# Performance work log

Measured on AMD Instinct MI355X. Metric: run time of the kernel, lower is better.

The kernel has to match this reference:

```python
import jax, jax.numpy as jnp
import numpy as np

B, S, D = 2, 4096, 512
H, DK, DV = 8, 64, 64
LN_EPS = 1e-5
ATTN_EPS = 1e-6


def layer_norm(x, g, b):
    mu = jnp.mean(x, axis=-1, keepdims=True)
    var = jnp.var(x, axis=-1, keepdims=True)
    return (x - mu) * jax.lax.rsqrt(var + LN_EPS) * g + b


def setup_inputs() -> dict:
    key = jax.random.key(0)
    ks = jax.random.split(key, 12)
    s = 1.0 / np.sqrt(D)
    inp = {
        "Q": jax.random.normal(ks[0], (B, S, D), jnp.float32),
        "K": jax.random.normal(ks[1], (B, S, D), jnp.float32),
        "V": jax.random.normal(ks[2], (B, S, D), jnp.float32),
        "W_q": jax.random.normal(ks[3], (D, H * DK), jnp.float32) * s,
        "W_k": jax.random.normal(ks[4], (D, H * DK), jnp.float32) * s,
        "W_v": jax.random.normal(ks[5], (D, H * DV), jnp.float32) * s,
        "W_o": jax.random.normal(ks[6], (H * DV, D), jnp.float32) * s,
        "ln1_g": jnp.ones((D,), jnp.float32),
        "ln1_b": jnp.zeros((D,), jnp.float32),
        "ln2_g": jnp.ones((D,), jnp.float32),
        "ln2_b": jnp.zeros((D,), jnp.float32),
        "w1": jax.random.normal(ks[7], (4 * D, D), jnp.float32) * s,  # torch Linear: (out, in)
        "b1": jnp.zeros((4 * D,), jnp.float32),
        "w2": jax.random.normal(ks[8], (D, 4 * D), jnp.float32) * (1.0 / np.sqrt(4 * D)),
        "b2": jnp.zeros((D,), jnp.float32),
    }
    return inp


def reference(Q, K, V, W_q, W_k, W_v, W_o, ln1_g, ln1_b, ln2_g, ln2_b, w1, b1, w2, b2):
    Qn = layer_norm(Q, ln1_g, ln1_b)
    # project and split heads: [B,S,H,dk] -> [B,H,S,dk]
    q = (Qn @ W_q).reshape(B, S, H, DK).transpose(0, 2, 1, 3)
    k = (K @ W_k).reshape(B, S, H, DK).transpose(0, 2, 1, 3)
    v = (V @ W_v).reshape(B, S, H, DV).transpose(0, 2, 1, 3)
    scores = jnp.einsum("bhqd,bhkd->bhqk", q, k) / (np.sqrt(DK) + ATTN_EPS)
    attn = jax.nn.softmax(scores, axis=-1)  # same as max-subtract softmax
    ctx = jnp.einsum("bhqk,bhkd->bhqd", attn, v)
    ctx = ctx.transpose(0, 2, 1, 3).reshape(B, S, H * DV)
    att_out = ctx @ W_o  # dropout = identity (eval)
    X = Q + att_out
    Xn = layer_norm(X, ln2_g, ln2_b)
    h = jax.nn.gelu(Xn @ w1.T + b1, approximate=False)
    ffn = h @ w2.T + b2
    return X + ffn
```

## Files before the change

kernel.cpp:

```cpp
#include <hip/hip_runtime.h>

typedef unsigned short u16;
typedef __attribute__((ext_vector_type(8))) short short8;
typedef __attribute__((ext_vector_type(4))) float f32x4;

struct __align__(8) us4 { u16 x, y, z, w; };
struct __align__(8) ui2 { unsigned x, y; };

#define CEXP (1.44269504089f / (8.0f + 1e-6f))

__device__ __forceinline__ u16 f2bf(float f) {
  unsigned u = __builtin_bit_cast(unsigned, f);
  unsigned r = (u + 0x7FFFu + ((u >> 16) & 1u)) >> 16;
  return (u16)r;
}

__device__ __forceinline__ unsigned pack_bf2_trunc(float a, float b) {
  return __builtin_amdgcn_perm(__builtin_bit_cast(unsigned, b),
                               __builtin_bit_cast(unsigned, a), 0x07060302u);
}

__device__ __forceinline__ void async_load16(const void* g, void* l) {
  __builtin_amdgcn_global_load_lds((const __attribute__((address_space(1))) void*)g,
                                   (__attribute__((address_space(3))) void*)l, 16, 0, 0);
}

__global__ void prep_weights(const float* __restrict__ Wq, const float* __restrict__ Wk,
                             const float* __restrict__ Wv, const float* __restrict__ Wo,
                             const float* __restrict__ w1, const float* __restrict__ w2,
                             u16* __restrict__ wqkvT, u16* __restrict__ woT,
                             u16* __restrict__ w1b, u16* __restrict__ w2b) {
  const int z = blockIdx.y;
  const int stride = gridDim.x * blockDim.x;
  const int i0 = blockIdx.x * blockDim.x + threadIdx.x;
  if (z < 4) {
    const float* src = z == 0 ? Wq : z == 1 ? Wk : z == 2 ? Wv : Wo;
    u16* dst = z < 3 ? wqkvT + z * 512 * 512 : woT;
    const float scale = (z == 0) ? CEXP : 1.0f;
    for (int i = i0; i < 512 * 512; i += stride) {
      int n = i >> 9, k = i & 511;
      dst[i] = f2bf(src[k * 512 + n] * scale);
    }
  } else {
    const float* src = z == 4 ? w1 : w2;
    u16* dst = z == 4 ? w1b : w2b;
    for (int i = i0; i < 2048 * 512; i += stride) dst[i] = f2bf(src[i]);
  }
}

template <bool KV>
__launch_bounds__(128)
__global__ void ln_cast(const float* __restrict__ X, const float* __restrict__ gw,
                        const float* __restrict__ bw, u16* __restrict__ Y,
                        const float* __restrict__ Kin, const float* __restrict__ Vin,
                        u16* __restrict__ Kb, u16* __restrict__ Vb) {
  const int row = blockIdx.x, t = threadIdx.x;
  const size_t base = (size_t)row * 512;
  float4 x = ((const float4*)(X + base))[t];
  float s = x.x + x.y + x.z + x.w;
  float ss = x.x * x.x + x.y * x.y + x.z * x.z + x.w * x.w;
#pragma unroll
  for (int off = 32; off > 0; off >>= 1) {
    s += __shfl_xor(s, off);
    ss += __shfl_xor(ss, off);
  }
  __shared__ float red[4];
  if ((t & 63) == 0) { red[(t >> 6) * 2] = s; red[(t >> 6) * 2 + 1] = ss; }
  __syncthreads();
  const float tot = red[0] + red[2], tss = red[1] + red[3];
  const float mu = tot * (1.0f / 512.0f);
  const float var = tss * (1.0f / 512.0f) - mu * mu;
  const float rs = rsqrtf(var + 1e-5f);
  float4 g4 = ((const float4*)gw)[t];
  float4 b4 = ((const float4*)bw)[t];
  us4 o;
  o.x = f2bf((x.x - mu) * rs * g4.x + b4.x);
  o.y = f2bf((x.y - mu) * rs * g4.y + b4.y);
  o.z = f2bf((x.z - mu) * rs * g4.z + b4.z);
  o.w = f2bf((x.w - mu) * rs * g4.w + b4.w);
  ((us4*)(Y + base))[t] = o;
  if constexpr (KV) {
    float4 k4 = ((const float4*)(Kin + base))[t];
    float4 v4 = ((const float4*)(Vin + base))[t];
    us4 ko, vo;
    ko.x = f2bf(k4.x); ko.y = f2bf(k4.y); ko.z = f2bf(k4.z); ko.w = f2bf(k4.w);
    vo.x = f2bf(v4.x); vo.y = f2bf(v4.y); vo.z = f2bf(v4.z); vo.w = f2bf(v4.w);
    ((us4*)(Kb + base))[t] = ko;
    ((us4*)(Vb + base))[t] = vo;
  }
}

__launch_bounds__(256, 3)
__global__ void gemm_qkv(const u16* __restrict__ Aq, const u16* __restrict__ Ak,
                         const u16* __restrict__ Av, const u16* __restrict__ Bt,
                         u16* __restrict__ qb, u16* __restrict__ kb, u16* __restrict__ vtb) {
  __shared__ __align__(16) u16 sA[128 * 32];
  __shared__ __align__(16) u16 sB[128 * 32];
  const int tid = threadIdx.x;
  const int wave = tid >> 6, lane = tid & 63;
  const int l15 = lane & 15, quad = lane >> 4;
  const int m0 = blockIdx.x * 128, n0 = blockIdx.y * 128;
  const int sel = n0 >> 9;
  const u16* A = sel == 0 ? Aq : sel == 1 ? Ak : Av;
  const int wm = (wave >> 1) * 64, wn = (wave & 1) * 64;
  const int u0 = wave * 64 + lane, u1 = u0 + 256;
  const int K = 512;

  const u16* a0 = A + (size_t)(m0 + (u0 >> 2)) * K + (u0 & 3) * 8;
  const u16* a1 = A + (size_t)(m0 + (u1 >> 2)) * K + (u1 & 3) * 8;
  const u16* b0 = Bt + (size_t)(n0 + (u0 >> 2)) * K + (u0 & 3) * 8;
  const u16* b1p = Bt + (size_t)(n0 + (u1 >> 2)) * K + (u1 & 3) * 8;

  f32x4 acc[4][4] = {};
  for (int k0 = 0; k0 < K; k0 += 32) {
    async_load16(a0 + k0, &sA[wave * 512]);
    async_load16(a1 + k0, &sA[2048 + wave * 512]);
    async_load16(b0 + k0, &sB[wave * 512]);
    async_load16(b1p + k0, &sB[2048 + wave * 512]);
    __syncthreads();
    short8 af[4], bfr[4];
#pragma unroll
    for (int i = 0; i < 4; i++)
      af[i] = *(const short8*)&sA[(wm + i * 16 + l15) * 32 + quad * 8];
#pragma unroll
    for (int j = 0; j < 4; j++)
      bfr[j] = *(const short8*)&sB[(wn + j * 16 + l15) * 32 + quad * 8];
#pragma unroll
    for (int i = 0; i < 4; i++)
#pragma unroll
      for (int j = 0; j < 4; j++)
        acc[i][j] = __builtin_amdgcn_mfma_f32_16x16x32_bf16(af[i], bfr[j], acc[i][j], 0, 0, 0);
    __syncthreads();
  }

#pragma unroll
  for (int i = 0; i < 4; i++) {
#pragma unroll
    for (int j = 0; j < 4; j++) {
      const int ocol = ((n0 + wn) & 511) + j * 16 + l15;
      const int row0 = m0 + wm + i * 16 + quad * 4;
      if (sel < 2) {
        u16* C = sel == 0 ? qb : kb;
#pragma unroll
        for (int r = 0; r < 4; r++) C[(size_t)(row0 + r) * 512 + ocol] = f2bf(acc[i][j][r]);
      } else {
        const int b = row0 >> 12, s0 = row0 & 4095;
        const int hh = ocol >> 6, cc = ocol & 63;
        us4 pk;
        pk.x = f2bf(acc[i][j][0]); pk.y = f2bf(acc[i][j][1]);
        pk.z = f2bf(acc[i][j][2]); pk.w = f2bf(acc[i][j][3]);
        *(us4*)&vtb[((size_t)((b * 8 + hh) * 64 + cc) << 12) + s0] = pk;
      }
    }
  }
}

template <int EP, int TN, int LB>
__launch_bounds__(256, LB)
__global__ void gemm_bt(const u16* __restrict__ A, const u16* __restrict__ Bt,
                        int M, int N, int K, void* __restrict__ Cp,
                        const float* __restrict__ bias, const float* __restrict__ res) {
  constexpr int MI = (TN == 128) ? 4 : 2;
  __shared__ __align__(16) u16 sA[128 * 32];
  __shared__ __align__(16) u16 sB[TN * 32];
  const int tid = threadIdx.x;
  const int wave = tid >> 6, lane = tid & 63;
  const int l15 = lane & 15, quad = lane >> 4;
  const int m0 = blockIdx.x * 128, n0 = blockIdx.y * TN;
  const int wm = (TN == 128) ? (wave >> 1) * 64 : wave * 32;
  const int wn = (TN == 128) ? (wave & 1) * 64 : 0;
  const int u0 = wave * 64 + lane, u1 = u0 + 256;

  const u16* a0 = A + (size_t)(m0 + (u0 >> 2)) * K + (u0 & 3) * 8;
  const u16* a1 = A + (size_t)(m0 + (u1 >> 2)) * K + (u1 & 3) * 8;
  const u16* b0 = Bt + (size_t)(n0 + (u0 >> 2)) * K + (u0 & 3) * 8;

  f32x4 acc[MI][4] = {};
  for (int k0 = 0; k0 < K; k0 += 32) {
    async_load16(a0 + k0, &sA[wave * 512]);
    async_load16(a1 + k0, &sA[2048 + wave * 512]);
    async_load16(b0 + k0, &sB[wave * 512]);
    if constexpr (TN == 128) {
      const u16* b1p = Bt + (size_t)(n0 + (u1 >> 2)) * K + (u1 & 3) * 8;
      async_load16(b1p + k0, &sB[2048 + wave * 512]);
    }
    __syncthreads();
    short8 af[MI], bfr[4];
#pragma unroll
    for (int i = 0; i < MI; i++)
      af[i] = *(const short8*)&sA[(wm + i * 16 + l15) * 32 + quad * 8];
#pragma unroll
    for (int j = 0; j < 4; j++)
      bfr[j] = *(const short8*)&sB[(wn + j * 16 + l15) * 32 + quad * 8];
#pragma unroll
    for (int i = 0; i < MI; i++)
#pragma unroll
      for (int j = 0; j < 4; j++)
        acc[i][j] = __builtin_amdgcn_mfma_f32_16x16x32_bf16(af[i], bfr[j], acc[i][j], 0, 0, 0);
    __syncthreads();
  }

#pragma unroll
  for (int i = 0; i < MI; i++) {
#pragma unroll
    for (int j = 0; j < 4; j++) {
      const int col = n0 + wn + j * 16 + l15;
      const int row0 = m0 + wm + i * 16 + quad * 4;
      if (EP == 2) {
        float* C = (float*)Cp;
#pragma unroll
        for (int r = 0; r < 4; r++) {
          size_t idx = (size_t)(row0 + r) * N + col;
          C[idx] = acc[i][j][r] + res[idx];
        }
      } else if (EP == 3) {
        u16* C = (u16*)Cp;
        const float bv = bias[col];
#pragma unroll
        for (int r = 0; r < 4; r++) {
          float xx = acc[i][j][r] + bv;
          float gl = 0.5f * xx * (1.0f + erff(xx * 0.70710678118f));
          C[(size_t)(row0 + r) * N + col] = f2bf(gl);
        }
      } else {
        float* C = (float*)Cp;
        const float bv = bias[col];
#pragma unroll
        for (int r = 0; r < 4; r++) {
          size_t idx = (size_t)(row0 + r) * N + col;
          C[idx] = acc[i][j][r] + bv + res[idx];
        }
      }
    }
  }
}

__launch_bounds__(256, 3)
__global__ void attn_kernel(const u16* __restrict__ qb, const u16* __restrict__ kb,
                            const u16* __restrict__ vtb, u16* __restrict__ ctx) {
  __shared__ __align__(16) u16 sK[2 * 128 * 32];
  __shared__ __align__(16) u16 sV[4 * 64 * 32];
  __shared__ __align__(16) u16 sP[4 * 32 * 40];
  const int tid = threadIdx.x;
  const int wave = tid >> 6, lane = tid & 63;
  const int l15 = lane & 15, quad = lane >> 4;
  const int bh = blockIdx.y, b = bh >> 3, h = bh & 7;
  const int q0 = blockIdx.x * 128;
  const size_t rb = (size_t)b * 4096;

  short8 qf[2][2];
#pragma unroll
  for (int mi = 0; mi < 2; mi++)
#pragma unroll
    for (int kk = 0; kk < 2; kk++) {
      int row = q0 + wave * 32 + mi * 16 + l15;
      qf[mi][kk] = *(const short8*)&qb[(rb + row) * 512 + h * 64 + kk * 32 + quad * 8];
    }

  f32x4 o_t[2][4] = {};
  float l_part[2] = {0.f, 0.f};
  u16* myP = &sP[wave * 32 * 40];

  for (int j0 = 0; j0 < 4096; j0 += 128) {
#pragma unroll
    for (int r = 0; r < 4; r++) {
      int u = r * 256 + wave * 64 + lane;
      int kk = u >> 9, key = (u >> 2) & 127, c8 = u & 3;
      async_load16(&kb[(rb + j0 + key) * 512 + h * 64 + kk * 32 + c8 * 8],
                   &sK[(r * 256 + wave * 64) * 8]);
    }
#pragma unroll
    for (int r = 0; r < 4; r++) {
      int u = r * 256 + wave * 64 + lane;
      int kk = u >> 8, vc = (u >> 2) & 63, c8 = u & 3;
      async_load16(&vtb[((size_t)(bh * 64 + vc)) * 4096 + j0 + kk * 32 + c8 * 8],
                   &sV[(r * 256 + wave * 64) * 8]);
    }
    __syncthreads();

#pragma unroll
    for (int kk = 0; kk < 4; kk++) {
#pragma unroll
      for (int nh = 0; nh < 2; nh++) {
        const int ni = kk * 2 + nh;
        short8 af0 = *(const short8*)&sK[(ni * 16 + l15) * 32 + quad * 8];
        short8 af1 = *(const short8*)&sK[4096 + (ni * 16 + l15) * 32 + quad * 8];
#pragma unroll
        for (int mi = 0; mi < 2; mi++) {
          f32x4 st = {};
          st = __builtin_amdgcn_mfma_f32_16x16x32_bf16(af0, qf[mi][0], st, 0, 0, 0);
          st = __builtin_amdgcn_mfma_f32_16x16x32_bf16(af1, qf[mi][1], st, 0, 0, 0);
          float p0 = exp2f(st[0]), p1 = exp2f(st[1]);
          float p2 = exp2f(st[2]), p3 = exp2f(st[3]);
          l_part[mi] += (p0 + p1) + (p2 + p3);
          ui2 w;
          w.x = pack_bf2_trunc(p0, p1);
          w.y = pack_bf2_trunc(p2, p3);
          *(ui2*)&myP[(mi * 16 + l15) * 40 + nh * 16 + quad * 4] = w;
        }
      }
      asm volatile("s_waitcnt lgkmcnt(0)" ::: "memory");
      short8 pf[2], vf[4];
#pragma unroll
      for (int mi = 0; mi < 2; mi++)
        pf[mi] = *(const short8*)&myP[(mi * 16 + l15) * 40 + quad * 8];
#pragma unroll
      for (int vi = 0; vi < 4; vi++)
        vf[vi] = *(const short8*)&sV[kk * 2048 + (vi * 16 + l15) * 32 + quad * 8];
#pragma unroll
      for (int mi = 0; mi < 2; mi++)
#pragma unroll
        for (int vi = 0; vi < 4; vi++)
          o_t[mi][vi] = __builtin_amdgcn_mfma_f32_16x16x32_bf16(vf[vi], pf[mi], o_t[mi][vi], 0, 0, 0);
    }
    __syncthreads();
  }

#pragma unroll
  for (int mi = 0; mi < 2; mi++) {
    float l = l_part[mi];
    l += __shfl_xor(l, 16);
    l += __shfl_xor(l, 32);
    const float inv = 1.0f / l;
    const int row = q0 + wave * 32 + mi * 16 + l15;
#pragma unroll
    for (int vi = 0; vi < 4; vi++) {
      us4 o;
      o.x = f2bf(o_t[mi][vi][0] * inv);
      o.y = f2bf(o_t[mi][vi][1] * inv);
      o.z = f2bf(o_t[mi][vi][2] * inv);
      o.w = f2bf(o_t[mi][vi][3] * inv);
      *(us4*)&ctx[(rb + row) * 512 + h * 64 + vi * 16 + quad * 4] = o;
    }
  }
}

extern "C" void kernel_launch(void* const* d_in, const int* in_sizes, int n_in,
                              void* d_out, int out_size, void* d_ws, size_t ws_size,
                              hipStream_t stream) {
  (void)in_sizes; (void)n_in; (void)out_size; (void)ws_size;
  const float* Q = (const float*)d_in[0];
  const float* K = (const float*)d_in[1];
  const float* V = (const float*)d_in[2];
  const float* W_q = (const float*)d_in[3];
  const float* W_k = (const float*)d_in[4];
  const float* W_v = (const float*)d_in[5];
  const float* W_o = (const float*)d_in[6];
  const float* ln1_g = (const float*)d_in[7];
  const float* ln1_b = (const float*)d_in[8];
  const float* ln2_g = (const float*)d_in[9];
  const float* ln2_b = (const float*)d_in[10];
  const float* w1 = (const float*)d_in[11];
  const float* b1 = (const float*)d_in[12];
  const float* w2 = (const float*)d_in[13];
  const float* b2 = (const float*)d_in[14];

  char* w = (char*)d_ws;
  const size_t MB = 1u << 20;
  u16* wqkvT = (u16*)(w);
  u16* woT = (u16*)(w + 3 * MB / 2);
  u16* w1b = (u16*)(w + 2 * MB);
  u16* w2b = (u16*)(w + 4 * MB);
  u16* Qn  = (u16*)(w + 6 * MB);
  u16* Kb  = (u16*)(w + 14 * MB);
  u16* Vb  = (u16*)(w + 22 * MB);
  u16* qb  = (u16*)(w + 30 * MB);
  u16* kb  = (u16*)(w + 38 * MB);
  u16* vtb = (u16*)(w + 46 * MB);
  u16* ctx = (u16*)(w + 54 * MB);
  float* X = (float*)(w + 62 * MB);
  u16* Xn  = (u16*)(w + 6 * MB);
  u16* hb  = (u16*)(w + 14 * MB);

  prep_weights<<<dim3(128, 6), 256, 0, stream>>>(W_q, W_k, W_v, W_o, w1, w2,
                                                 wqkvT, woT, w1b, w2b);
  ln_cast<true><<<8192, 128, 0, stream>>>(Q, ln1_g, ln1_b, Qn, K, V, Kb, Vb);
  gemm_qkv<<<dim3(64, 12), 256, 0, stream>>>(Qn, Kb, Vb, wqkvT, qb, kb, vtb);
  attn_kernel<<<dim3(32, 16), 256, 0, stream>>>(qb, kb, vtb, ctx);
  gemm_bt<2, 64, 3><<<dim3(64, 8), 256, 0, stream>>>(ctx, woT, 8192, 512, 512, X, nullptr, Q);
  ln_cast<false><<<8192, 128, 0, stream>>>(X, ln2_g, ln2_b, Xn, nullptr, nullptr, nullptr, nullptr);
  gemm_bt<3, 128, 3><<<dim3(64, 16), 256, 0, stream>>>(Xn, w1b, 8192, 2048, 512, hb, b1, nullptr);
  gemm_bt<4, 64, 3><<<dim3(64, 8), 256, 0, stream>>>(hb, w2b, 8192, 512, 2048, (float*)d_out, b2, X);
}
```

Before: 369.9 us.

## Swizzle LDS tiles to avoid bank conflicts and shrink attention query tile

Applies an XOR swizzle on the 16-byte chunk index when staging A/B tiles and K/V tiles into LDS, with a matching swizzle on the fragment reads, to reduce LDS bank conflicts. The attention kernel now handles 64 queries per block (16 per wave) instead of 128, doubling the grid and raising launch bounds to 4 blocks per SM. It also uses the raw hardware exp2 intrinsic. Smaller query tiles increase parallelism and cut registers, but K/V tiles are reloaded twice as often.

```diff
diff --git a/kernel.cpp b/kernel.cpp
--- a/kernel.cpp
+++ b/kernel.cpp
@@ -99,17 +99,19 @@
   const int tid = threadIdx.x;
   const int wave = tid >> 6, lane = tid & 63;
   const int l15 = lane & 15, quad = lane >> 4;
+  const int qsw = (quad ^ ((l15 >> 1) & 3)) * 8;
   const int m0 = blockIdx.x * 128, n0 = blockIdx.y * 128;
   const int sel = n0 >> 9;
   const u16* A = sel == 0 ? Aq : sel == 1 ? Ak : Av;
   const int wm = (wave >> 1) * 64, wn = (wave & 1) * 64;
   const int u0 = wave * 64 + lane, u1 = u0 + 256;
+  const int sw0 = ((u0 & 3) ^ ((u0 >> 3) & 3)) * 8;
   const int K = 512;
 
-  const u16* a0 = A + (size_t)(m0 + (u0 >> 2)) * K + (u0 & 3) * 8;
-  const u16* a1 = A + (size_t)(m0 + (u1 >> 2)) * K + (u1 & 3) * 8;
-  const u16* b0 = Bt + (size_t)(n0 + (u0 >> 2)) * K + (u0 & 3) * 8;
-  const u16* b1p = Bt + (size_t)(n0 + (u1 >> 2)) * K + (u1 & 3) * 8;
+  const u16* a0 = A + (size_t)(m0 + (u0 >> 2)) * K + sw0;
+  const u16* a1 = A + (size_t)(m0 + (u1 >> 2)) * K + sw0;
+  const u16* b0 = Bt + (size_t)(n0 + (u0 >> 2)) * K + sw0;
+  const u16* b1p = Bt + (size_t)(n0 + (u1 >> 2)) * K + sw0;
 
   f32x4 acc[4][4] = {};
   for (int k0 = 0; k0 < K; k0 += 32) {
@@ -121,10 +123,10 @@
     short8 af[4], bfr[4];
 #pragma unroll
     for (int i = 0; i < 4; i++)
-      af[i] = *(const short8*)&sA[(wm + i * 16 + l15) * 32 + quad * 8];
+      af[i] = *(const short8*)&sA[(wm + i * 16 + l15) * 32 + qsw];
 #pragma unroll
     for (int j = 0; j < 4; j++)
-      bfr[j] = *(const short8*)&sB[(wn + j * 16 + l15) * 32 + quad * 8];
+      bfr[j] = *(const short8*)&sB[(wn + j * 16 + l15) * 32 + qsw];
 #pragma unroll
     for (int i = 0; i < 4; i++)
 #pragma unroll
@@ -166,14 +168,16 @@
   const int tid = threadIdx.x;
   const int wave = tid >> 6, lane = tid & 63;
   const int l15 = lane & 15, quad = lane >> 4;
+  const int qsw = (quad ^ ((l15 >> 1) & 3)) * 8;
   const int m0 = blockIdx.x * 128, n0 = blockIdx.y * TN;
   const int wm = (TN == 128) ? (wave >> 1) * 64 : wave * 32;
   const int wn = (TN == 128) ? (wave & 1) * 64 : 0;
   const int u0 = wave * 64 + lane, u1 = u0 + 256;
-
-  const u16* a0 = A + (size_t)(m0 + (u0 >> 2)) * K + (u0 & 3) * 8;
-  const u16* a1 = A + (size_t)(m0 + (u1 >> 2)) * K + (u1 & 3) * 8;
-  const u16* b0 = Bt + (size_t)(n0 + (u0 >> 2)) * K + (u0 & 3) * 8;
+  const int sw0 = ((u0 & 3) ^ ((u0 >> 3) & 3)) * 8;
+
+  const u16* a0 = A + (size_t)(m0 + (u0 >> 2)) * K + sw0;
+  const u16* a1 = A + (size_t)(m0 + (u1 >> 2)) * K + sw0;
+  const u16* b0 = Bt + (size_t)(n0 + (u0 >> 2)) * K + sw0;
 
   f32x4 acc[MI][4] = {};
   for (int k0 = 0; k0 < K; k0 += 32) {
@@ -181,17 +185,17 @@
     async_load16(a1 + k0, &sA[2048 + wave * 512]);
     async_load16(b0 + k0, &sB[wave * 512]);
     if constexpr (TN == 128) {
-      const u16* b1p = Bt + (size_t)(n0 + (u1 >> 2)) * K + (u1 & 3) * 8;
+      const u16* b1p = Bt + (size_t)(n0 + (u1 >> 2)) * K + sw0;
       async_load16(b1p + k0, &sB[2048 + wave * 512]);
     }
     __syncthreads();
     short8 af[MI], bfr[4];
 #pragma unroll
     for (int i = 0; i < MI; i++)
-      af[i] = *(const short8*)&sA[(wm + i * 16 + l15) * 32 + quad * 8];
+      af[i] = *(const short8*)&sA[(wm + i * 16 + l15) * 32 + qsw];
 #pragma unroll
     for (int j = 0; j < 4; j++)
-      bfr[j] = *(const short8*)&sB[(wn + j * 16 + l15) * 32 + quad * 8];
+      bfr[j] = *(const short8*)&sB[(wn + j * 16 + l15) * 32 + qsw];
 #pragma unroll
     for (int i = 0; i < MI; i++)
 #pragma unroll
@@ -235,44 +239,42 @@
   }
 }
 
-__launch_bounds__(256, 3)
+__launch_bounds__(256, 4)
 __global__ void attn_kernel(const u16* __restrict__ qb, const u16* __restrict__ kb,
                             const u16* __restrict__ vtb, u16* __restrict__ ctx) {
   __shared__ __align__(16) u16 sK[2 * 128 * 32];
   __shared__ __align__(16) u16 sV[4 * 64 * 32];
-  __shared__ __align__(16) u16 sP[4 * 32 * 40];
+  __shared__ __align__(16) u16 sP[4 * 16 * 40];
   const int tid = threadIdx.x;
   const int wave = tid >> 6, lane = tid & 63;
   const int l15 = lane & 15, quad = lane >> 4;
+  const int qsw = (quad ^ ((l15 >> 1) & 3)) * 8;
   const int bh = blockIdx.y, b = bh >> 3, h = bh & 7;
-  const int q0 = blockIdx.x * 128;
+  const int q0 = blockIdx.x * 64;
   const size_t rb = (size_t)b * 4096;
-
-  short8 qf[2][2];
-#pragma unroll
-  for (int mi = 0; mi < 2; mi++)
-#pragma unroll
-    for (int kk = 0; kk < 2; kk++) {
-      int row = q0 + wave * 32 + mi * 16 + l15;
-      qf[mi][kk] = *(const short8*)&qb[(rb + row) * 512 + h * 64 + kk * 32 + quad * 8];
-    }
-
-  f32x4 o_t[2][4] = {};
-  float l_part[2] = {0.f, 0.f};
-  u16* myP = &sP[wave * 32 * 40];
+  const int qrow = q0 + wave * 16 + l15;
+
+  short8 qf[2];
+#pragma unroll
+  for (int kk = 0; kk < 2; kk++)
+    qf[kk] = *(const short8*)&qb[(rb + qrow) * 512 + h * 64 + kk * 32 + quad * 8];
+
+  f32x4 o_t[4] = {};
+  float l_part = 0.f;
+  u16* myP = &sP[wave * 16 * 40];
 
   for (int j0 = 0; j0 < 4096; j0 += 128) {
 #pragma unroll
     for (int r = 0; r < 4; r++) {
       int u = r * 256 + wave * 64 + lane;
-      int kk = u >> 9, key = (u >> 2) & 127, c8 = u & 3;
+      int kk = u >> 9, key = (u >> 2) & 127, c8 = (u & 3) ^ ((u >> 3) & 3);
       async_load16(&kb[(rb + j0 + key) * 512 + h * 64 + kk * 32 + c8 * 8],
                    &sK[(r * 256 + wave * 64) * 8]);
     }
 #pragma unroll
     for (int r = 0; r < 4; r++) {
       int u = r * 256 + wave * 64 + lane;
-      int kk = u >> 8, vc = (u >> 2) & 63, c8 = u & 3;
+      int kk = u >> 8, vc = (u >> 2) & 63, c8 = (u & 3) ^ ((u >> 3) & 3);
       async_load16(&vtb[((size_t)(bh * 64 + vc)) * 4096 + j0 + kk * 32 + c8 * 8],
                    &sV[(r * 256 + wave * 64) * 8]);
     }
@@ -283,55 +285,46 @@
 #pragma unroll
       for (int nh = 0; nh < 2; nh++) {
         const int ni = kk * 2 + nh;
-        short8 af0 = *(const short8*)&sK[(ni * 16 + l15) * 32 + quad * 8];
-        short8 af1 = *(const short8*)&sK[4096 + (ni * 16 + l15) * 32 + quad * 8];
-#pragma unroll
-        for (int mi = 0; mi < 2; mi++) {
-          f32x4 st = {};
-          st = __builtin_amdgcn_mfma_f32_16x16x32_bf16(af0, qf[mi][0], st, 0, 0, 0);
-          st = __builtin_amdgcn_mfma_f32_16x16x32_bf16(af1, qf[mi][1], st, 0, 0, 0);
-          float p0 = exp2f(st[0]), p1 = exp2f(st[1]);
-          float p2 = exp2f(st[2]), p3 = exp2f(st[3]);
-          l_part[mi] += (p0 + p1) + (p2 + p3);
-          ui2 w;
-          w.x = pack_bf2_trunc(p0, p1);
-          w.y = pack_bf2_trunc(p2, p3);
-          *(ui2*)&myP[(mi * 16 + l15) * 40 + nh * 16 + quad * 4] = w;
-        }
+        short8 af0 = *(const short8*)&sK[(ni * 16 + l15) * 32 + qsw];
+        short8 af1 = *(const short8*)&sK[4096 + (ni * 16 + l15) * 32 + qsw];
+        f32x4 st = {};
+        st = __builtin_amdgcn_mfma_f32_16x16x32_bf16(af0, qf[0], st, 0, 0, 0);
+        st = __builtin_amdgcn_mfma_f32_16x16x32_bf16(af1, qf[1], st, 0, 0, 0);
+        float p0 = __builtin_amdgcn_exp2f(st[0]);
+        float p1 = __builtin_amdgcn_exp2f(st[1]);
+        float p2 = __builtin_amdgcn_exp2f(st[2]);
+        float p3 = __builtin_amdgcn_exp2f(st[3]);
+        l_part += (p0 + p1) + (p2 + p3);
+        ui2 w;
+        w.x = pack_bf2_trunc(p0, p1);
+        w.y = pack_bf2_trunc(p2, p3);
+        *(ui2*)&myP[l15 * 40 + nh * 16 + quad * 4] = w;
       }
       asm volatile("s_waitcnt lgkmcnt(0)" ::: "memory");
-      short8 pf[2], vf[4];
-#pragma unroll
-      for (int mi = 0; mi < 2; mi++)
-        pf[mi] = *(const short8*)&myP[(mi * 16 + l15) * 40 + quad * 8];
+      short8 pf = *(const short8*)&myP[l15 * 40 + quad * 8];
+      short8 vf[4];
 #pragma unroll
       for (int vi = 0; vi < 4; vi++)
-        vf[vi] = *(const short8*)&sV[kk * 2048 + (vi * 16 + l15) * 32 + quad * 8];
-#pragma unroll
-      for (int mi = 0; mi < 2; mi++)
-#pragma unroll
-        for (int vi = 0; vi < 4; vi++)
-          o_t[mi][vi] = __builtin_amdgcn_mfma_f32_16x16x32_bf16(vf[vi], pf[mi], o_t[mi][vi], 0, 0, 0);
-    }
-    __syncthreads();
-  }
-
-#pragma unroll
-  for (int mi = 0; mi < 2; mi++) {
-    float l = l_part[mi];
-    l += __shfl_xor(l, 16);
-    l += __shfl_xor(l, 32);
-    const float inv = 1.0f / l;
-    const int row = q0 + wave * 32 + mi * 16 + l15;
-#pragma unroll
-    for (int vi = 0; vi < 4; vi++) {
-      us4 o;
-      o.x = f2bf(o_t[mi][vi][0] * inv);
-      o.y = f2bf(o_t[mi][vi][1] * inv);
-      o.z = f2bf(o_t[mi][vi][2] * inv);
-      o.w = f2bf(o_t[mi][vi][3] * inv);
-      *(us4*)&ctx[(rb + row) * 512 + h * 64 + vi * 16 + quad * 4] = o;
-    }
+        vf[vi] = *(const short8*)&sV[kk * 2048 + (vi * 16 + l15) * 32 + qsw];
+#pragma unroll
+      for (int vi = 0; vi < 4; vi++)
+        o_t[vi] = __builtin_amdgcn_mfma_f32_16x16x32_bf16(vf[vi], pf, o_t[vi], 0, 0, 0);
+    }
+    __syncthreads();
+  }
+
+  float l = l_part;
+  l += __shfl_xor(l, 16);
+  l += __shfl_xor(l, 32);
+  const float inv = 1.0f / l;
+#pragma unroll
+  for (int vi = 0; vi < 4; vi++) {
+    us4 o;
+    o.x = f2bf(o_t[vi][0] * inv);
+    o.y = f2bf(o_t[vi][1] * inv);
+    o.z = f2bf(o_t[vi][2] * inv);
+    o.w = f2bf(o_t[vi][3] * inv);
+    *(us4*)&ctx[(rb + qrow) * 512 + h * 64 + vi * 16 + quad * 4] = o;
   }
 }
 
@@ -376,7 +369,7 @@
                                                  wqkvT, woT, w1b, w2b);
   ln_cast<true><<<8192, 128, 0, stream>>>(Q, ln1_g, ln1_b, Qn, K, V, Kb, Vb);
   gemm_qkv<<<dim3(64, 12), 256, 0, stream>>>(Qn, Kb, Vb, wqkvT, qb, kb, vtb);
-  attn_kernel<<<dim3(32, 16), 256, 0, stream>>>(qb, kb, vtb, ctx);
+  attn_kernel<<<dim3(64, 16), 256, 0, stream>>>(qb, kb, vtb, ctx);
   gemm_bt<2, 64, 3><<<dim3(64, 8), 256, 0, stream>>>(ctx, woT, 8192, 512, 512, X, nullptr, Q);
   ln_cast<false><<<8192, 128, 0, stream>>>(X, ln2_g, ln2_b, Xn, nullptr, nullptr, nullptr, nullptr);
   gemm_bt<3, 128, 3><<<dim3(64, 16), 256, 0, stream>>>(Xn, w1b, 8192, 2048, 512, hb, b1, nullptr);
```

Result: faster. 344.2 us (-7.0%).
